# Kernel optimization log

Hardware: AMD Instinct MI355X
Metric: run time of the kernel (lower is better)

The kernel has to match this reference:

```python
import jax, jax.numpy as jnp
import numpy as np

B, DM, NH, NL, NP = 4, 768, 12, 3, 4
HD = DM // NH
H_IMG, W_IMG = 896, 896
LEVELS = [(H_IMG // 8, W_IMG // 8), (H_IMG // 16, W_IMG // 16), (H_IMG // 32, W_IMG // 32)]
QH, QW = H_IMG // 14, W_IMG // 14
LQ = QH * QW            # 4096 query tokens (stride-14 ViT grid)
LIN = sum(h * w for h, w in LEVELS)  # 16464 multi-scale value tokens


def setup_inputs() -> dict:
    key = jax.random.key(0)
    ks = jax.random.split(key, 14)
    s = 0.02
    return {
        "query": jax.random.normal(ks[0], (B, LQ, DM), jnp.float32),
        "feat": jax.random.normal(ks[1], (B, LIN, DM), jnp.float32),
        "ln_q_g": jnp.ones((DM,), jnp.float32),
        "ln_q_b": jnp.zeros((DM,), jnp.float32),
        "ln_f_g": jnp.ones((DM,), jnp.float32),
        "ln_f_b": jnp.zeros((DM,), jnp.float32),
        "W_off": jax.random.normal(ks[2], (DM, NH * NL * NP * 2), jnp.float32) * s,
        "b_off": jax.random.normal(ks[3], (NH * NL * NP * 2,), jnp.float32) * s,
        "W_attn": jax.random.normal(ks[4], (DM, NH * NL * NP), jnp.float32) * s,
        "b_attn": jax.random.normal(ks[5], (NH * NL * NP,), jnp.float32) * s,
        "W_val": jax.random.normal(ks[6], (DM, DM), jnp.float32) * s,
        "b_val": jnp.zeros((DM,), jnp.float32),
        "W_out": jax.random.normal(ks[7], (DM, DM), jnp.float32) * s,
        "b_out": jnp.zeros((DM,), jnp.float32),
        "gamma": jax.random.normal(ks[8], (DM,), jnp.float32) * s,
    }


def _ln(x, g, b, eps=1e-6):
    m = x.mean(-1, keepdims=True)
    v = ((x - m) ** 2).mean(-1, keepdims=True)
    return (x - m) * jax.lax.rsqrt(v + eps) * g + b


def _ref_points():
    # get_reference_points for the stride-14 query grid; pixel-center coords normalized
    ry, rx = jnp.meshgrid(
        (jnp.arange(QH, dtype=jnp.float32) + 0.5) / QH,
        (jnp.arange(QW, dtype=jnp.float32) + 0.5) / QW,
        indexing="ij",
    )
    return jnp.stack([rx.reshape(-1), ry.reshape(-1)], -1)  # (LQ, 2) in (x, y)


def _sample_level(v, loc, h_, w_):
    # v: (B, h_, w_, NH, HD); loc: (B, LQ, NH, NP, 2) normalized [0,1]
    # torch grid_sample bilinear, align_corners=False, zero padding
    x = loc[..., 0] * w_ - 0.5
    y = loc[..., 1] * h_ - 0.5
    x0 = jnp.floor(x)
    y0 = jnp.floor(y)
    wx = (x - x0)[..., None]
    wy = (y - y0)[..., None]
    x0i = x0.astype(jnp.int32)
    y0i = y0.astype(jnp.int32)
    bi = jnp.arange(B)[:, None, None, None]
    hi = jnp.arange(NH)[None, None, :, None]

    def g(yi, xi):
        valid = ((xi >= 0) & (xi < w_) & (yi >= 0) & (yi < h_)).astype(v.dtype)
        got = v[bi, jnp.clip(yi, 0, h_ - 1), jnp.clip(xi, 0, w_ - 1), hi]  # (B,LQ,NH,NP,HD)
        return got * valid[..., None]

    v00 = g(y0i, x0i)
    v01 = g(y0i, x0i + 1)
    v10 = g(y0i + 1, x0i)
    v11 = g(y0i + 1, x0i + 1)
    return v00 * (1 - wx) * (1 - wy) + v01 * wx * (1 - wy) + v10 * (1 - wx) * wy + v11 * wx * wy


def _injector(query, feat, ln_q_g, ln_q_b, ln_f_g, ln_f_b, W_off, b_off, W_attn, b_attn,
              W_val, b_val, W_out, b_out, gamma):
    q = _ln(query, ln_q_g, ln_q_b)
    f = _ln(feat, ln_f_g, ln_f_b)
    value = (f @ W_val + b_val).reshape(B, LIN, NH, HD)
    off = (q @ W_off + b_off).reshape(B, LQ, NH, NL, NP, 2)
    aw = jax.nn.softmax((q @ W_attn + b_attn).reshape(B, LQ, NH, NL * NP), axis=-1)
    aw = aw.reshape(B, LQ, NH, NL, NP)
    ref = _ref_points()  # (LQ, 2)
    offset_norm = jnp.array([[w, h] for h, w in LEVELS], jnp.float32)  # (NL, 2) = (W_, H_)
    loc = ref[None, :, None, None, None, :] + off / offset_norm[None, None, None, :, None, :]
    outs = []
    start = 0
    for lvl, (h_, w_) in enumerate(LEVELS):
        v = value[:, start:start + h_ * w_].reshape(B, h_, w_, NH, HD)
        outs.append(_sample_level(v, loc[:, :, :, lvl], h_, w_))
        start += h_ * w_
    samp = jnp.stack(outs, axis=3)  # (B, LQ, NH, NL, NP, HD)
    attn_out = (samp * aw[..., None]).sum(axis=(3, 4)).reshape(B, LQ, DM)
    attn_out = attn_out @ W_out + b_out
    return query + gamma * attn_out


def reference(query, feat, ln_q_g, ln_q_b, ln_f_g, ln_f_b, W_off, b_off, W_attn, b_attn,
              W_val, b_val, W_out, b_out, gamma):
    return _injector(query, feat, ln_q_g, ln_q_b, ln_f_g, ln_f_b, W_off, b_off, W_attn,
                     b_attn, W_val, b_val, W_out, b_out, gamma)
```

## Files before the change

kernel.cpp:

```cpp
#include <hip/hip_runtime.h>
#include <hip/hip_bf16.h>

typedef __hip_bfloat16 bf16;

#define BB    4
#define LQ    4096
#define LIN   16464
#define DM    768
#define NH    12
#define HD    64
#define K_DIM 768

typedef __attribute__((ext_vector_type(8))) __bf16 bfrag;
typedef __attribute__((ext_vector_type(4))) float  ffrag;

__device__ __forceinline__ void g2l16(const void* g, void* l) {
    __builtin_amdgcn_global_load_lds(
        (const __attribute__((address_space(1))) void*)g,
        (__attribute__((address_space(3))) void*)l, 16, 0, 0);
}

__device__ __forceinline__ int xcd_swz(int orig, int nwg) {
    int xcd = orig & 7, within = orig >> 3;
    int q = nwg >> 3, r = nwg & 7;
    return (xcd < r ? xcd * (q + 1) : r * (q + 1) + (xcd - r) * q) + within;
}

__global__ __launch_bounds__(256) void ln_kernel(
    const float* __restrict__ x, const float* __restrict__ g,
    const float* __restrict__ beta, bf16* __restrict__ y)
{
    int r = blockIdx.x * 4 + (threadIdx.x >> 6);
    int lane = threadIdx.x & 63;
    const float4* xr = (const float4*)(x + (size_t)r * DM);
    float4 v[3];
    #pragma unroll
    for (int i = 0; i < 3; i++) v[i] = xr[lane + 64 * i];
    float s = 0.f, ss = 0.f;
    #pragma unroll
    for (int i = 0; i < 3; i++) {
        s  += v[i].x + v[i].y + v[i].z + v[i].w;
        ss += v[i].x * v[i].x + v[i].y * v[i].y + v[i].z * v[i].z + v[i].w * v[i].w;
    }
    #pragma unroll
    for (int m = 1; m <= 32; m <<= 1) {
        s  += __shfl_xor(s, m);
        ss += __shfl_xor(ss, m);
    }
    float mean = s * (1.f / DM);
    float inv  = rsqrtf(ss * (1.f / DM) - mean * mean + 1e-6f);
    bf16* yr = y + (size_t)r * DM;
    #pragma unroll
    for (int i = 0; i < 3; i++) {
        float4 gg = ((const float4*)g)[lane + 64 * i];
        float4 bb = ((const float4*)beta)[lane + 64 * i];
        union { bf16 h[4]; uint2 u; } p;
        p.h[0] = __float2bfloat16((v[i].x - mean) * inv * gg.x + bb.x);
        p.h[1] = __float2bfloat16((v[i].y - mean) * inv * gg.y + bb.y);
        p.h[2] = __float2bfloat16((v[i].z - mean) * inv * gg.z + bb.z);
        p.h[3] = __float2bfloat16((v[i].w - mean) * inv * gg.w + bb.w);
        *(uint2*)(yr + (lane + 64 * i) * 4) = p.u;
    }
}

__global__ __launch_bounds__(256) void cast_transpose(
    const float* __restrict__ W, bf16* __restrict__ Wt, int N)
{
    __shared__ float t[32][33];
    int n0 = blockIdx.x * 32, k0 = blockIdx.y * 32;
    int tx = threadIdx.x & 31, ty = threadIdx.x >> 5;
    #pragma unroll
    for (int i = 0; i < 4; i++) {
        int k = k0 + ty + i * 8;
        int n = n0 + tx;
        t[ty + i * 8][tx] = (n < N) ? W[(size_t)k * N + n] : 0.f;
    }
    __syncthreads();
    #pragma unroll
    for (int i = 0; i < 4; i++) {
        int n = n0 + ty + i * 8;
        Wt[(size_t)n * K_DIM + k0 + tx] = __float2bfloat16(t[tx][ty + i * 8]);
    }
}

__device__ __forceinline__ void gemm_epilogue(
    ffrag acc[4][4], int bm, int bn, int wr, int wc, int lane,
    const float* bias, void* C, const float* resid, const float* gamma,
    const float* bias2, int M, int N, int mode, int nsplit)
{
    int mrow = lane & 15;
    int q4 = (lane >> 4) * 4;
    #pragma unroll
    for (int i = 0; i < 4; i++) {
        #pragma unroll
        for (int rr = 0; rr < 4; rr++) {
            int rg = bm + wr + i * 16 + q4 + rr;
            if (rg < M) {
                #pragma unroll
                for (int j = 0; j < 4; j++) {
                    int cg = bn + wc + j * 16 + mrow;
                    if (cg < N) {
                        float bv = (mode == 3 && cg >= nsplit) ? bias2[cg - nsplit]
                                                               : bias[cg];
                        float v = acc[i][j][rr] + bv;
                        size_t idx = (size_t)rg * N + cg;
                        if (mode == 0)      ((bf16*)C)[idx]  = __float2bfloat16(v);
                        else if (mode == 2) ((float*)C)[idx] = resid[idx] + gamma[cg] * v;
                        else                ((float*)C)[idx] = v;
                    }
                }
            }
        }
    }
}

template<int TAG>
__global__ __launch_bounds__(256) void mfma_gemm_t(
    const bf16*  __restrict__ A,
    const bf16*  __restrict__ Bt,
    const float* __restrict__ bias,
    void*        __restrict__ C,
    const float* __restrict__ resid,
    const float* __restrict__ gamma,
    const float* __restrict__ bias2,
    int M, int N, int mode, int nsplit)
{
    __shared__ __align__(16) char lds[32768];

    int tid  = threadIdx.x;
    int lane = tid & 63;

    int nwg  = gridDim.x * gridDim.y;
    int orig = blockIdx.y * gridDim.x + blockIdx.x;
    int wg = xcd_swz(orig, nwg);
    int bn = (wg % gridDim.x) * 128;
    int bm = (wg / gridDim.x) * 128;

    int wave = tid >> 6;
    int wr = (wave & 1) * 64, wc = (wave >> 1) * 64;

    ffrag acc[4][4] = {};

    int rA = tid >> 2;
    int kb = (((tid & 3) ^ ((rA >> 1) & 3)) * 8);
    int ra0 = min(bm + rA, M - 1), ra1 = min(bm + 64 + rA, M - 1);
    const bf16* gA0 = A  + (size_t)ra0 * K_DIM + kb;
    const bf16* gA1 = A  + (size_t)ra1 * K_DIM + kb;
    const bf16* gB0 = Bt + (size_t)(bn + rA) * K_DIM + kb;
    const bf16* gB1 = Bt + (size_t)(bn + 64 + rA) * K_DIM + kb;

    int mrow = lane & 15;
    int kqs  = (((lane >> 4) ^ ((mrow >> 1) & 3)) * 8);

    auto stage = [&](char* buf, int kt) {
        const int ko = kt * 32;
        g2l16(gA0 + ko, buf + tid * 16);
        g2l16(gA1 + ko, buf + tid * 16 + 4096);
        g2l16(gB0 + ko, buf + 8192 + tid * 16);
        g2l16(gB1 + ko, buf + 8192 + tid * 16 + 4096);
    };

    stage(lds, 0);
    asm volatile("s_waitcnt vmcnt(0)" ::: "memory");
    __builtin_amdgcn_s_barrier();

    #pragma unroll
    for (int kt = 0; kt < 24; kt++) {
        char* cur = lds + (kt & 1) * 16384;
        char* nxt = lds + ((kt & 1) ^ 1) * 16384;
        if (kt + 1 < 24) stage(nxt, kt + 1);

        bfrag a[4], b[4];
        #pragma unroll
        for (int t = 0; t < 4; t++) {
            a[t] = *(const bfrag*)(cur + ((wr + t * 16 + mrow) * 32 + kqs) * 2);
            b[t] = *(const bfrag*)(cur + 8192 + ((wc + t * 16 + mrow) * 32 + kqs) * 2);
        }
        __builtin_amdgcn_s_setprio(1);
        #pragma unroll
        for (int i = 0; i < 4; i++)
            #pragma unroll
            for (int j = 0; j < 4; j++)
                acc[i][j] = __builtin_amdgcn_mfma_f32_16x16x32_bf16(
                    a[i], b[j], acc[i][j], 0, 0, 0);
        __builtin_amdgcn_s_setprio(0);

        asm volatile("s_waitcnt vmcnt(0)" ::: "memory");
        __builtin_amdgcn_s_barrier();
    }

    gemm_epilogue(acc, bm, bn, wr, wc, lane, bias, C, resid, gamma, bias2,
                  M, N, mode, nsplit);
}

__global__ __launch_bounds__(256) void sample_kernel(
    const bf16*  __restrict__ value,
    const float* __restrict__ comb,
    bf16*        __restrict__ attn)
{
    int wg = xcd_swz(blockIdx.x, gridDim.x);
    int unit = __builtin_amdgcn_readfirstlane((wg << 2) + (threadIdx.x >> 6));
    int lane = threadIdx.x & 63;
    int o   = lane & 7;
    int c8  = lane >> 3;
    int k   = c8 & 3;
    int dx  = k & 1, dy = k >> 1;
    int h  = unit % NH;
    int bq = unit / NH;
    int q  = bq & (LQ - 1);
    int b  = bq >> 12;

    const float* rowp = comb + (size_t)bq * 432;
    const float* ob = rowp + h * 24;
    const float* lg = rowp + 288 + h * 12;

    float l[12];
    float mx = -1e30f;
    #pragma unroll
    for (int i = 0; i < 12; i++) { l[i] = lg[i]; mx = fmaxf(mx, l[i]); }
    float den = 0.f;
    #pragma unroll
    for (int i = 0; i < 12; i++) { l[i] = __expf(l[i] - mx); den += l[i]; }
    float rden = 1.f / den;
    #pragma unroll
    for (int i = 0; i < 12; i++) l[i] *= rden;

    float rx = ((q & 63) + 0.5f) * (1.f / 64.f);
    float ry = ((q >> 6) + 0.5f) * (1.f / 64.f);

    float acc[8] = {0.f};

    #pragma unroll
    for (int it = 0; it < 6; it++) {
        const int wl = (it < 2) ? 112 : (it < 4 ? 56 : 28);
        const int sl = (it < 2) ? 0   : (it < 4 ? 12544 : 15680);
        int s = it * 2 + ((lane >> 5) & 1);
        float ox = ob[s * 2 + 0];
        float oy = ob[s * 2 + 1];
        float x = rx * wl + ox - 0.5f;
        float y = ry * wl + oy - 0.5f;
        float xf = floorf(x), yf = floorf(y);
        float wx = x - xf,  wy = y - yf;
        int xi = (int)xf + dx;
        int yi = (int)yf + dy;
        bool valid = ((unsigned)xi < (unsigned)wl) & ((unsigned)yi < (unsigned)wl);
        int xc = min(max(xi, 0), wl - 1);
        int yc = min(max(yi, 0), wl - 1);
        int cell = b * LIN + sl + yc * wl + xc;
        const uint4* vp = (const uint4*)(value + ((size_t)cell * NH + h) * HD + o * 8);
        uint4 v = *vp;
        float aw = (lane & 32) ? l[it * 2 + 1] : l[it * 2];
        float bw = (dx ? wx : 1.f - wx) * (dy ? wy : 1.f - wy);
        float w = valid ? aw * bw : 0.f;
        const unsigned* u = (const unsigned*)&v;
        #pragma unroll
        for (int j = 0; j < 4; j++) {
            float f0 = __uint_as_float(u[j] << 16);
            float f1 = __uint_as_float(u[j] & 0xFFFF0000u);
            acc[j * 2 + 0] = fmaf(w, f0, acc[j * 2 + 0]);
            acc[j * 2 + 1] = fmaf(w, f1, acc[j * 2 + 1]);
        }
    }

    #pragma unroll
    for (int m = 8; m <= 32; m <<= 1) {
        #pragma unroll
        for (int j = 0; j < 8; j++)
            acc[j] += __shfl_xor(acc[j], m);
    }

    if (c8 == 0) {
        union { bf16 h8[8]; uint4 u4; } r;
        #pragma unroll
        for (int j = 0; j < 8; j++) r.h8[j] = __float2bfloat16(acc[j]);
        *(uint4*)(attn + (size_t)bq * DM + h * HD + o * 8) = r.u4;
    }
}

extern "C" void kernel_launch(void* const* d_in, const int* in_sizes, int n_in,
                              void* d_out, int out_size, void* d_ws, size_t ws_size,
                              hipStream_t stream)
{
    const float* query  = (const float*)d_in[0];
    const float* feat   = (const float*)d_in[1];
    const float* ln_q_g = (const float*)d_in[2];
    const float* ln_q_b = (const float*)d_in[3];
    const float* ln_f_g = (const float*)d_in[4];
    const float* ln_f_b = (const float*)d_in[5];
    const float* W_off  = (const float*)d_in[6];
    const float* b_off  = (const float*)d_in[7];
    const float* W_attn = (const float*)d_in[8];
    const float* b_attn = (const float*)d_in[9];
    const float* W_val  = (const float*)d_in[10];
    const float* b_val  = (const float*)d_in[11];
    const float* W_out  = (const float*)d_in[12];
    const float* b_out  = (const float*)d_in[13];
    const float* gamma  = (const float*)d_in[14];
    float* out = (float*)d_out;

    char* ws = (char*)d_ws;
    char* od = (char*)d_out;
    const int M_F = BB * LIN;
    const int M_Q = BB * LQ;

    bf16*  value  = (bf16*)(ws);
    bf16*  f_ln   = (bf16*)(ws + 101154816);
    bf16*  Wt_out = (bf16*)(ws + 101154816);
    bf16*  q_ln   = (bf16*)(ws + 202309632);
    bf16*  attn   = (bf16*)(ws + 202309632);

    bf16*  Wt_val  = (bf16*)(od);
    bf16*  Wt_comb = (bf16*)(od + 1179648);
    float* comb    = (float*)(od + 2162688);

    cast_transpose<<<dim3(24, 24), 256, 0, stream>>>(W_val, Wt_val, 768);
    cast_transpose<<<dim3(9, 24), 256, 0, stream>>>(W_off, Wt_comb, 288);
    cast_transpose<<<dim3(7, 24), 256, 0, stream>>>(
        W_attn, Wt_comb + (size_t)288 * K_DIM, 144);

    ln_kernel<<<M_F / 4, 256, 0, stream>>>(feat, ln_f_g, ln_f_b, f_ln);
    ln_kernel<<<M_Q / 4, 256, 0, stream>>>(query, ln_q_g, ln_q_b, q_ln);

    mfma_gemm_t<0><<<dim3(6, (M_F + 127) / 128), 256, 0, stream>>>(
        f_ln, Wt_val, b_val, value, nullptr, nullptr, nullptr, M_F, DM, 0, 0);

    cast_transpose<<<dim3(24, 24), 256, 0, stream>>>(W_out, Wt_out, 768);

    mfma_gemm_t<1><<<dim3(4, M_Q / 128), 256, 0, stream>>>(
        q_ln, Wt_comb, b_off, comb, nullptr, nullptr, b_attn, M_Q, 432, 3, 288);

    sample_kernel<<<(M_Q * NH) / 4, 256, 0, stream>>>(value, comb, attn);

    mfma_gemm_t<2><<<dim3(6, M_Q / 128), 256, 0, stream>>>(
        attn, Wt_out, b_out, out, query, gamma, nullptr, M_Q, DM, 2, 0);
}
```

Measured before the change: 771.5 us.

## Use 256x256 tiled 8-wave GEMM with staged quarter prefetch for value projection

Replaces the 128x128 value-projection GEMM with a 512-thread kernel computing 256x256 tiles, BK=64 and 128KB double-buffered LDS. Prefetch of the next k-tile is split into four quarter stages interleaved with MFMA sub-blocks, so loads overlap compute. The larger tile raises arithmetic intensity and cuts global traffic for the largest GEMM (M=65856). The cost is fewer workgroups (3x258), low occupancy, higher register pressure and a tail on the partial last M tile. The remaining GEMMs are split into mode-specific wrappers around a shared body.

```diff
diff --git a/kernel.cpp b/kernel.cpp
--- a/kernel.cpp
+++ b/kernel.cpp
@@ -83,12 +83,222 @@
     }
 }
 
-__device__ __forceinline__ void gemm_epilogue(
-    ffrag acc[4][4], int bm, int bn, int wr, int wc, int lane,
-    const float* bias, void* C, const float* resid, const float* gamma,
-    const float* bias2, int M, int N, int mode, int nsplit)
-{
+__global__ __launch_bounds__(512) void gemm256_value(
+    const bf16*  __restrict__ A,
+    const bf16*  __restrict__ Bt,
+    const float* __restrict__ bias,
+    bf16*        __restrict__ C,
+    int M, int N)
+{
+    __shared__ __align__(16) char lds[131072];
+
+    int tid  = threadIdx.x;
+    int lane = tid & 63;
+    int wave = tid >> 6;
+
+    int nwg  = gridDim.x * gridDim.y;
+    int orig = blockIdx.y * gridDim.x + blockIdx.x;
+    int wg   = xcd_swz(orig, nwg);
+    int bn = (wg % gridDim.x) * 256;
+    int bm = (wg / gridDim.x) * 256;
+
+    int ahalf = wave >> 2;
+    int wc    = (wave & 3) * 64;
+    int bhalf = (wave & 3) >> 1;
+    int bcb   = (wave & 1) * 64;
+
+    int ln15 = lane & 15, g = lane >> 4, l7 = lane & 7;
+
+    ffrag acc[8][4] = {};
+
+    int r_loc = tid >> 3;
+    int koff  = (((tid & 7) ^ (r_loc & 7)) * 8);
+
+    const bf16* gA[2][2];
+    const bf16* gB[2][2];
+    #pragma unroll
+    for (int h = 0; h < 2; h++)
+        #pragma unroll
+        for (int ld = 0; ld < 2; ld++) {
+            int ra = min(bm + h * 128 + ld * 64 + r_loc, M - 1);
+            gA[h][ld] = A  + (size_t)ra * K_DIM + koff;
+            int cb = bn + h * 128 + ld * 64 + r_loc;
+            gB[h][ld] = Bt + (size_t)cb * K_DIM + koff;
+        }
+
+    auto stageA = [&](char* buf, int h, int kt) {
+        g2l16(gA[h][0] + kt * 64, buf + h * 16384 + tid * 16);
+        g2l16(gA[h][1] + kt * 64, buf + h * 16384 + 8192 + tid * 16);
+    };
+    auto stageB = [&](char* buf, int h, int kt) {
+        g2l16(gB[h][0] + kt * 64, buf + 32768 + h * 16384 + tid * 16);
+        g2l16(gB[h][1] + kt * 64, buf + 32768 + h * 16384 + 8192 + tid * 16);
+    };
+
+    stageA(lds, 0, 0); stageA(lds, 1, 0); stageB(lds, 0, 0); stageB(lds, 1, 0);
+
+    int sby[2];
+    sby[0] = ((0 * 4 + g) ^ l7) * 16;
+    sby[1] = ((1 * 4 + g) ^ l7) * 16;
+
+    #pragma unroll
+    for (int kt = 0; kt < 12; kt++) {
+        char* cur = lds + (kt & 1) * 65536;
+        char* nxt = lds + ((kt & 1) ^ 1) * 65536;
+        const char* Ac = cur + ahalf * 16384;
+        const char* Bc = cur + 32768 + bhalf * 16384;
+
+        if (kt + 1 < 12) {
+            stageA(nxt, 0, kt + 1);
+            asm volatile("s_waitcnt vmcnt(2)" ::: "memory");
+        } else {
+            asm volatile("s_waitcnt vmcnt(0)" ::: "memory");
+        }
+        __builtin_amdgcn_s_barrier();
+
+        bfrag bf[4][2];
+        #pragma unroll
+        for (int nc = 0; nc < 4; nc++)
+            #pragma unroll
+            for (int ks = 0; ks < 2; ks++)
+                bf[nc][ks] = *(const bfrag*)(Bc + (bcb + nc * 16 + ln15) * 128 + sby[ks]);
+        {
+            bfrag af[2][2];
+            #pragma unroll
+            for (int m2 = 0; m2 < 2; m2++)
+                #pragma unroll
+                for (int ks = 0; ks < 2; ks++)
+                    af[m2][ks] = *(const bfrag*)(Ac + (m2 * 16 + ln15) * 128 + sby[ks]);
+            __builtin_amdgcn_s_setprio(1);
+            #pragma unroll
+            for (int m2 = 0; m2 < 2; m2++)
+                #pragma unroll
+                for (int nc = 0; nc < 4; nc++)
+                    #pragma unroll
+                    for (int ks = 0; ks < 2; ks++)
+                        acc[m2][nc] = __builtin_amdgcn_mfma_f32_16x16x32_bf16(
+                            af[m2][ks], bf[nc][ks], acc[m2][nc], 0, 0, 0);
+            __builtin_amdgcn_s_setprio(0);
+        }
+        __builtin_amdgcn_s_barrier();
+
+        #pragma unroll
+        for (int qd = 1; qd < 4; qd++) {
+            if (kt + 1 < 12) {
+                if (qd == 1) stageA(nxt, 1, kt + 1);
+                else if (qd == 2) stageB(nxt, 0, kt + 1);
+                else stageB(nxt, 1, kt + 1);
+            }
+            bfrag af[2][2];
+            #pragma unroll
+            for (int m2 = 0; m2 < 2; m2++)
+                #pragma unroll
+                for (int ks = 0; ks < 2; ks++)
+                    af[m2][ks] = *(const bfrag*)(Ac + ((qd * 2 + m2) * 16 + ln15) * 128 + sby[ks]);
+            __builtin_amdgcn_s_setprio(1);
+            #pragma unroll
+            for (int m2 = 0; m2 < 2; m2++)
+                #pragma unroll
+                for (int nc = 0; nc < 4; nc++)
+                    #pragma unroll
+                    for (int ks = 0; ks < 2; ks++)
+                        acc[qd * 2 + m2][nc] = __builtin_amdgcn_mfma_f32_16x16x32_bf16(
+                            af[m2][ks], bf[nc][ks], acc[qd * 2 + m2][nc], 0, 0, 0);
+            __builtin_amdgcn_s_setprio(0);
+            __builtin_amdgcn_s_barrier();
+        }
+    }
+
+    int q4 = g * 4;
+    #pragma unroll
+    for (int mr = 0; mr < 8; mr++) {
+        #pragma unroll
+        for (int rr = 0; rr < 4; rr++) {
+            int rg = bm + ahalf * 128 + mr * 16 + q4 + rr;
+            if (rg < M) {
+                #pragma unroll
+                for (int nc = 0; nc < 4; nc++) {
+                    int cg = bn + wc + nc * 16 + ln15;
+                    C[(size_t)rg * N + cg] =
+                        __float2bfloat16(acc[mr][nc][rr] + bias[cg]);
+                }
+            }
+        }
+    }
+}
+
+__device__ __forceinline__ void gemm128_body(
+    const bf16*  __restrict__ A,
+    const bf16*  __restrict__ Bt,
+    const float* __restrict__ bias,
+    void*        __restrict__ C,
+    const float* __restrict__ resid,
+    const float* __restrict__ gamma,
+    const float* __restrict__ bias2,
+    int M, int N, int mode, int nsplit, char* lds)
+{
+    int tid  = threadIdx.x;
+    int lane = tid & 63;
+
+    int nwg  = gridDim.x * gridDim.y;
+    int orig = blockIdx.y * gridDim.x + blockIdx.x;
+    int wg = xcd_swz(orig, nwg);
+    int bn = (wg % gridDim.x) * 128;
+    int bm = (wg / gridDim.x) * 128;
+
+    int wave = tid >> 6;
+    int wr = (wave & 1) * 64, wc = (wave >> 1) * 64;
+
+    ffrag acc[4][4] = {};
+
+    int rA = tid >> 2;
+    int kb = (((tid & 3) ^ ((rA >> 1) & 3)) * 8);
+    int ra0 = min(bm + rA, M - 1), ra1 = min(bm + 64 + rA, M - 1);
+    const bf16* gA0 = A  + (size_t)ra0 * K_DIM + kb;
+    const bf16* gA1 = A  + (size_t)ra1 * K_DIM + kb;
+    const bf16* gB0 = Bt + (size_t)(bn + rA) * K_DIM + kb;
+    const bf16* gB1 = Bt + (size_t)(bn + 64 + rA) * K_DIM + kb;
+
     int mrow = lane & 15;
+    int kqs  = (((lane >> 4) ^ ((mrow >> 1) & 3)) * 8);
+
+    auto stage = [&](char* buf, int kt) {
+        const int ko = kt * 32;
+        g2l16(gA0 + ko, buf + tid * 16);
+        g2l16(gA1 + ko, buf + tid * 16 + 4096);
+        g2l16(gB0 + ko, buf + 8192 + tid * 16);
+        g2l16(gB1 + ko, buf + 8192 + tid * 16 + 4096);
+    };
+
+    stage(lds, 0);
+    asm volatile("s_waitcnt vmcnt(0)" ::: "memory");
+    __builtin_amdgcn_s_barrier();
+
+    #pragma unroll
+    for (int kt = 0; kt < 24; kt++) {
+        char* cur = lds + (kt & 1) * 16384;
+        char* nxt = lds + ((kt & 1) ^ 1) * 16384;
+        if (kt + 1 < 24) stage(nxt, kt + 1);
+
+        bfrag a[4], b[4];
+        #pragma unroll
+        for (int t = 0; t < 4; t++) {
+            a[t] = *(const bfrag*)(cur + ((wr + t * 16 + mrow) * 32 + kqs) * 2);
+            b[t] = *(const bfrag*)(cur + 8192 + ((wc + t * 16 + mrow) * 32 + kqs) * 2);
+        }
+        __builtin_amdgcn_s_setprio(1);
+        #pragma unroll
+        for (int i = 0; i < 4; i++)
+            #pragma unroll
+            for (int j = 0; j < 4; j++)
+                acc[i][j] = __builtin_amdgcn_mfma_f32_16x16x32_bf16(
+                    a[i], b[j], acc[i][j], 0, 0, 0);
+        __builtin_amdgcn_s_setprio(0);
+
+        asm volatile("s_waitcnt vmcnt(0)" ::: "memory");
+        __builtin_amdgcn_s_barrier();
+    }
+
     int q4 = (lane >> 4) * 4;
     #pragma unroll
     for (int i = 0; i < 4; i++) {
@@ -104,8 +314,7 @@
                                                                : bias[cg];
                         float v = acc[i][j][rr] + bv;
                         size_t idx = (size_t)rg * N + cg;
-                        if (mode == 0)      ((bf16*)C)[idx]  = __float2bfloat16(v);
-                        else if (mode == 2) ((float*)C)[idx] = resid[idx] + gamma[cg] * v;
+                        if (mode == 2)      ((float*)C)[idx] = resid[idx] + gamma[cg] * v;
                         else                ((float*)C)[idx] = v;
                     }
                 }
@@ -114,83 +323,23 @@
     }
 }
 
-template<int TAG>
-__global__ __launch_bounds__(256) void mfma_gemm_t(
-    const bf16*  __restrict__ A,
-    const bf16*  __restrict__ Bt,
-    const float* __restrict__ bias,
-    void*        __restrict__ C,
-    const float* __restrict__ resid,
-    const float* __restrict__ gamma,
-    const float* __restrict__ bias2,
-    int M, int N, int mode, int nsplit)
+__global__ __launch_bounds__(256) void gemm128_comb(
+    const bf16* __restrict__ A, const bf16* __restrict__ Bt,
+    const float* __restrict__ bias, void* __restrict__ C,
+    const float* __restrict__ bias2, int M, int N, int nsplit)
 {
     __shared__ __align__(16) char lds[32768];
-
-    int tid  = threadIdx.x;
-    int lane = tid & 63;
-
-    int nwg  = gridDim.x * gridDim.y;
-    int orig = blockIdx.y * gridDim.x + blockIdx.x;
-    int wg = xcd_swz(orig, nwg);
-    int bn = (wg % gridDim.x) * 128;
-    int bm = (wg / gridDim.x) * 128;
-
-    int wave = tid >> 6;
-    int wr = (wave & 1) * 64, wc = (wave >> 1) * 64;
-
-    ffrag acc[4][4] = {};
-
-    int rA = tid >> 2;
-    int kb = (((tid & 3) ^ ((rA >> 1) & 3)) * 8);
-    int ra0 = min(bm + rA, M - 1), ra1 = min(bm + 64 + rA, M - 1);
-    const bf16* gA0 = A  + (size_t)ra0 * K_DIM + kb;
-    const bf16* gA1 = A  + (size_t)ra1 * K_DIM + kb;
-    const bf16* gB0 = Bt + (size_t)(bn + rA) * K_DIM + kb;
-    const bf16* gB1 = Bt + (size_t)(bn + 64 + rA) * K_DIM + kb;
-
-    int mrow = lane & 15;
-    int kqs  = (((lane >> 4) ^ ((mrow >> 1) & 3)) * 8);
-
-    auto stage = [&](char* buf, int kt) {
-        const int ko = kt * 32;
-        g2l16(gA0 + ko, buf + tid * 16);
-        g2l16(gA1 + ko, buf + tid * 16 + 4096);
-        g2l16(gB0 + ko, buf + 8192 + tid * 16);
-        g2l16(gB1 + ko, buf + 8192 + tid * 16 + 4096);
-    };
-
-    stage(lds, 0);
-    asm volatile("s_waitcnt vmcnt(0)" ::: "memory");
-    __builtin_amdgcn_s_barrier();
-
-    #pragma unroll
-    for (int kt = 0; kt < 24; kt++) {
-        char* cur = lds + (kt & 1) * 16384;
-        char* nxt = lds + ((kt & 1) ^ 1) * 16384;
-        if (kt + 1 < 24) stage(nxt, kt + 1);
-
-        bfrag a[4], b[4];
-        #pragma unroll
-        for (int t = 0; t < 4; t++) {
-            a[t] = *(const bfrag*)(cur + ((wr + t * 16 + mrow) * 32 + kqs) * 2);
-            b[t] = *(const bfrag*)(cur + 8192 + ((wc + t * 16 + mrow) * 32 + kqs) * 2);
-        }
-        __builtin_amdgcn_s_setprio(1);
-        #pragma unroll
-        for (int i = 0; i < 4; i++)
-            #pragma unroll
-            for (int j = 0; j < 4; j++)
-                acc[i][j] = __builtin_amdgcn_mfma_f32_16x16x32_bf16(
-                    a[i], b[j], acc[i][j], 0, 0, 0);
-        __builtin_amdgcn_s_setprio(0);
-
-        asm volatile("s_waitcnt vmcnt(0)" ::: "memory");
-        __builtin_amdgcn_s_barrier();
-    }
-
-    gemm_epilogue(acc, bm, bn, wr, wc, lane, bias, C, resid, gamma, bias2,
-                  M, N, mode, nsplit);
+    gemm128_body(A, Bt, bias, C, nullptr, nullptr, bias2, M, N, 3, nsplit, lds);
+}
+
+__global__ __launch_bounds__(256) void gemm128_out(
+    const bf16* __restrict__ A, const bf16* __restrict__ Bt,
+    const float* __restrict__ bias, void* __restrict__ C,
+    const float* __restrict__ resid, const float* __restrict__ gamma,
+    int M, int N)
+{
+    __shared__ __align__(16) char lds[32768];
+    gemm128_body(A, Bt, bias, C, resid, gamma, nullptr, M, N, 2, 0, lds);
 }
 
 __global__ __launch_bounds__(256) void sample_kernel(
@@ -321,16 +470,16 @@
     ln_kernel<<<M_F / 4, 256, 0, stream>>>(feat, ln_f_g, ln_f_b, f_ln);
     ln_kernel<<<M_Q / 4, 256, 0, stream>>>(query, ln_q_g, ln_q_b, q_ln);
 
-    mfma_gemm_t<0><<<dim3(6, (M_F + 127) / 128), 256, 0, stream>>>(
-        f_ln, Wt_val, b_val, value, nullptr, nullptr, nullptr, M_F, DM, 0, 0);
+    gemm256_value<<<dim3(3, (M_F + 255) / 256), 512, 0, stream>>>(
+        f_ln, Wt_val, b_val, value, M_F, DM);
 
     cast_transpose<<<dim3(24, 24), 256, 0, stream>>>(W_out, Wt_out, 768);
 
-    mfma_gemm_t<1><<<dim3(4, M_Q / 128), 256, 0, stream>>>(
-        q_ln, Wt_comb, b_off, comb, nullptr, nullptr, b_attn, M_Q, 432, 3, 288);
+    gemm128_comb<<<dim3(4, M_Q / 128), 256, 0, stream>>>(
+        q_ln, Wt_comb, b_off, comb, b_attn, M_Q, 432, 288);
 
     sample_kernel<<<(M_Q * NH) / 4, 256, 0, stream>>>(value, comb, attn);
 
-    mfma_gemm_t<2><<<dim3(6, M_Q / 128), 256, 0, stream>>>(
-        attn, Wt_out, b_out, out, query, gamma, nullptr, M_Q, DM, 2, 0);
-}
+    gemm128_out<<<dim3(6, M_Q / 128), 256, 0, stream>>>(
+        attn, Wt_out, b_out, out, query, gamma, M_Q, DM);
+}
```

Result: faster. 702.6 us (-8.9%).
